# Performance work log

Hardware: AMD Instinct MI355X
Metric: run time of the kernel (lower is better)

Reference implementation:

```python
import math
import jax, jax.numpy as jnp
import numpy as np

N = 50000
C = 128      # in_channels == out_channels
H = 8        # nhead
D = C // H   # head_dim = 16
E = 800000


def _layernorm(x, g, b, eps=1e-5):
    mu = jnp.mean(x, axis=-1, keepdims=True)
    var = jnp.var(x, axis=-1, keepdims=True)
    return (x - mu) * jax.lax.rsqrt(var + eps) * g + b


def setup_inputs() -> dict:
    key = jax.random.key(0)
    ks = jax.random.split(key, 12)
    s = 1.0 / math.sqrt(C)          # ~xavier scale
    s4 = 1.0 / math.sqrt(4 * C)
    return {
        "x": jax.random.normal(ks[0], (N, C), dtype=jnp.float32),
        "edge_index": jax.random.randint(ks[1], (2, E), 0, N, dtype=jnp.int64),
        "Wq": jax.random.normal(ks[2], (C, C), dtype=jnp.float32) * s,
        "Wk": jax.random.normal(ks[3], (C, C), dtype=jnp.float32) * s,
        "Wv": jax.random.normal(ks[4], (C, C), dtype=jnp.float32) * s,
        "Wo": jax.random.normal(ks[5], (C, C), dtype=jnp.float32) * s,
        "bo": jnp.zeros((C,), dtype=jnp.float32),
        "Wf1": jax.random.normal(ks[6], (C, 4 * C), dtype=jnp.float32) * s,
        "bf1": jnp.zeros((4 * C,), dtype=jnp.float32),
        "Wf2": jax.random.normal(ks[7], (4 * C, C), dtype=jnp.float32) * s4,
        "bf2": jnp.zeros((C,), dtype=jnp.float32),
        "g1": jnp.ones((C,), dtype=jnp.float32),
        "b1": jnp.zeros((C,), dtype=jnp.float32),
        "g2": jnp.ones((C,), dtype=jnp.float32),
        "b2": jnp.zeros((C,), dtype=jnp.float32),
    }


def reference(x, edge_index, Wq, Wk, Wv, Wo, bo, Wf1, bf1, Wf2, bf2, g1, b1, g2, b2):
    n = x.shape[0]
    loops = jnp.arange(n, dtype=edge_index.dtype)
    row = jnp.concatenate([edge_index[0], loops])  # source nodes
    col = jnp.concatenate([edge_index[1], loops])  # destination nodes

    q = (x @ Wq).reshape(n, H, D)
    k = (x @ Wk).reshape(n, H, D)
    v = (x @ Wv).reshape(n, H, D)

    # edge-level attention scores [E+N, H]
    scores = jnp.einsum('ehd,ehd->eh', q[row], k[col]) / math.sqrt(D)
    smax = jax.ops.segment_max(scores, col, num_segments=n)  # every node has a self-loop
    exp = jnp.exp(scores - smax[col])
    ssum = jax.ops.segment_sum(exp, col, num_segments=n)
    alpha = exp / (ssum[col] + 1e-8)

    out = jax.ops.segment_sum(v[row] * alpha[..., None], col, num_segments=n)
    attn = out.reshape(n, C) @ Wo + bo

    residual = x  # input_proj is Identity (in_channels == out_channels)
    x1 = _layernorm(residual + attn, g1, b1)
    ffn = jax.nn.gelu(x1 @ Wf1 + bf1, approximate=False) @ Wf2 + bf2
    return _layernorm(x1 + ffn, g2, b2)
```

## Files before the change

kernel.cpp:

```cpp
#include <hip/hip_runtime.h>
#include <cmath>


typedef short bf16x8 __attribute__((ext_vector_type(8)));
typedef float f32x4 __attribute__((ext_vector_type(4)));
typedef unsigned int uint_as1 __attribute__((address_space(1)));
typedef unsigned int uint_as3 __attribute__((address_space(3)));

__device__ inline unsigned short f2bf(float f) {
    unsigned int u = __float_as_uint(f);
    u += 0x7fffu + ((u >> 16) & 1u);
    return (unsigned short)(u >> 16);
}
__device__ inline float bflo(unsigned int w) { return __uint_as_float(w << 16); }
__device__ inline float bfhi(unsigned int w) { return __uint_as_float(w & 0xffff0000u); }

__device__ inline void gload16(const unsigned short* g, unsigned short* l) {
    __builtin_amdgcn_global_load_lds((const uint_as1*)g, (uint_as3*)l, 16, 0, 0);
}

__device__ inline float gelu_f(float x) {
    float ax = fabsf(x) * 0.70710678118f;
    float t = __builtin_amdgcn_rcpf(fmaf(0.3275911f, ax, 1.0f));
    float p = fmaf(1.061405429f, t, -1.453152027f);
    p = fmaf(p, t, 1.421413741f);
    p = fmaf(p, t, -0.284496736f);
    p = fmaf(p, t, 0.254829592f);
    p = p * t;
    float e = __expf(-ax * ax);
    float pe = p * e;
    float w = (x >= 0.f) ? (2.0f - pe) : pe;
    return 0.5f * x * w;
}


__device__ __forceinline__ void stage_panel(unsigned short* Bs,
                                            const unsigned short* base,
                                            int strideK) {
    int tid = threadIdx.x;
    int srow = tid >> 4, cc = tid & 15;
    int gc = (cc & ~7) | ((cc & 7) ^ (srow & 7));
    const unsigned short* src = base + (size_t)srow * strideK + gc * 8;
    unsigned short* dst = Bs + srow * 128 + cc * 8;
#pragma unroll
    for (int j = 0; j < 8; ++j)
        gload16(src + (size_t)j * 16 * strideK, dst + j * 16 * 128);
}

__device__ __forceinline__ void loadA16(bf16x8 (&af)[4],
                                        const unsigned short* A, int M, int K,
                                        int base, int ko, int l16, int quad) {
    int row = base + l16;
    if (row > M - 1) row = M - 1;
    const unsigned short* ar = A + (size_t)row * K + ko + quad * 8;
#pragma unroll
    for (int j = 0; j < 4; ++j) af[j] = *(const bf16x8*)(ar + j * 32);
}

__device__ __forceinline__ void loadA_k(bf16x8 (&af)[4][4],
                                        const unsigned short* A, int M, int K,
                                        int m0, int ko, int wr, int l16, int quad) {
#pragma unroll
    for (int ti = 0; ti < 4; ++ti) {
        int row = m0 + wr * 64 + ti * 16 + l16;
        if (row > M - 1) row = M - 1;
        const unsigned short* ar = A + (size_t)row * K + ko + quad * 8;
#pragma unroll
        for (int j = 0; j < 4; ++j) af[ti][j] = *(const bf16x8*)(ar + j * 32);
    }
}

__device__ __forceinline__ void mm16(f32x4 (&acc)[4][4], const bf16x8 (&af)[4][4],
                                     const unsigned short* Bs,
                                     int wc, int quad, int l16) {
#pragma unroll
    for (int ks = 0; ks < 4; ++ks) {
        bf16x8 bfr[4];
#pragma unroll
        for (int tj = 0; tj < 4; ++tj) {
            int nr = wc * 64 + tj * 16 + l16;
            int cidx = ks * 4 + quad;
            int slot = (cidx & ~7) | ((cidx & 7) ^ (nr & 7));
            bfr[tj] = *(const bf16x8*)&Bs[nr * 128 + slot * 8];
        }
#pragma unroll
        for (int ti = 0; ti < 4; ++ti)
#pragma unroll
            for (int tj = 0; tj < 4; ++tj)
                acc[ti][tj] = __builtin_amdgcn_mfma_f32_16x16x32_bf16(
                    af[ti][ks], bfr[tj], acc[ti][tj], 0, 0, 0);
    }
}


__global__ __launch_bounds__(256) void k_init(
    const float* __restrict__ x, unsigned short* __restrict__ xb,
    const float* __restrict__ Wq, const float* __restrict__ Wk,
    const float* __restrict__ Wv, const float* __restrict__ Wo,
    const float* __restrict__ Wf1, const float* __restrict__ Wf2,
    unsigned short* __restrict__ Wqkvt, unsigned short* __restrict__ Wot,
    unsigned short* __restrict__ Wf1t, unsigned short* __restrict__ Wf2t,
    int* __restrict__ cursor, int4* __restrict__ csrz,
    int N, int nCsr4, int nCast) {
    int bid = blockIdx.x;
    int t = threadIdx.x;

    int NBc = (N + 255) >> 8;
    if (bid < NBc) {
        int i = bid * 256 + t;
        if (i < N) cursor[i] = 0;
        return;
    }
    bid -= NBc;
    int NBz = (nCsr4 + 255) >> 8;
    if (bid < NBz) {
        int i = bid * 256 + t;
        if (i < nCsr4) csrz[i] = make_int4(0, 0, 0, 0);
        return;
    }
    bid -= NBz;
    if (bid < nCast) {
        int i = bid * 256 + t;
        if (i < N * 32) {
            float4 v = ((const float4*)x)[i];
            ushort4 o;
            o.x = f2bf(v.x); o.y = f2bf(v.y); o.z = f2bf(v.z); o.w = f2bf(v.w);
            ((ushort4*)xb)[i] = o;
        }
        return;
    }
    bid -= nCast;
    int z, idx;
    if (bid < 256) { z = bid >> 6; idx = (bid & 63) * 256 + t; }
    else           { z = 4 + ((bid - 256) >> 8); idx = ((bid - 256) & 255) * 256 + t; }

    const float* in; unsigned short* out; int K, Co;
    switch (z) {
        case 0: in = Wq;  out = Wqkvt; K = 128; Co = 128; break;
        case 1: in = Wk;  out = Wqkvt; K = 128; Co = 128; break;
        case 2: in = Wv;  out = Wqkvt; K = 128; Co = 128; break;
        case 3: in = Wo;  out = Wot;   K = 128; Co = 128; break;
        case 4: in = Wf1; out = Wf1t;  K = 128; Co = 512; break;
        default: in = Wf2; out = Wf2t; K = 512; Co = 128; break;
    }
    if (idx >= K * Co) return;
    int k = idx / Co, c = idx % Co;
    int row;
    switch (z) {
        case 0: row = ((c >> 1) << 2) | (c & 1); break;
        case 1: row = 256 + c; break;
        case 2: row = (((c >> 1) << 2) | (c & 1)) + 2; break;
        default: row = c; break;
    }
    out[(size_t)row * K + k] = f2bf(in[idx]);
}


__global__ void k_fill(const int* __restrict__ ei, int* __restrict__ cursor,
                       unsigned short* __restrict__ csr, int E, int N) {
    int e = blockIdx.x * 256 + threadIdx.x;
    if (e >= E + N) return;
    int row, col;
    if (e < E) { row = ei[e]; col = ei[E + e]; }
    else       { row = col = e - E; }
    int pos = atomicAdd(&cursor[col], 1);
    csr[(size_t)col * 64 + pos] = (unsigned short)row;
}


template <int EPI>
__global__ __launch_bounds__(256) void k_gemmP(
    const unsigned short* __restrict__ A, const unsigned short* __restrict__ Bt,
    const float* __restrict__ bias, const float* __restrict__ resid,
    const float* __restrict__ g, const float* __restrict__ b,
    float* __restrict__ outf, unsigned short* __restrict__ outb,
    int M, int Cout, int NZ) {
    __shared__ unsigned short Bs[128 * 128];

    int tid = threadIdx.x;
    int w = tid >> 6, lane = tid & 63;
    int quad = lane >> 4, l16 = lane & 15;
    int zi = blockIdx.x % NZ;
    int ci = blockIdx.x / NZ;
    int n0 = zi * 128;

    stage_panel(Bs, Bt + (size_t)n0 * 128, 128);

    float bi[8], gv[8], bv[8];
    if constexpr (EPI >= 1) {
#pragma unroll
        for (int tj = 0; tj < 8; ++tj) bi[tj] = bias[n0 * (EPI == 1) + tj * 16 + l16];
    }
    if constexpr (EPI == 2) {
#pragma unroll
        for (int tj = 0; tj < 8; ++tj) {
            gv[tj] = g[tj * 16 + l16];
            bv[tj] = b[tj * 16 + l16];
        }
    }

    int base0 = ci * 128 + w * 16;
    int base1 = base0 + 64;
    bf16x8 afA[4], afB[4];
    loadA16(afA, A, M, 128, base0, 0, l16, quad);
    loadA16(afB, A, M, 128, base1, 0, l16, quad);
    __syncthreads();

    auto tile = [&](const bf16x8 (&af)[4], int base) {
        f32x4 acc[8];
#pragma unroll
        for (int tj = 0; tj < 8; ++tj) acc[tj] = {0.f, 0.f, 0.f, 0.f};
#pragma unroll
        for (int ks = 0; ks < 4; ++ks) {
            int cidx = ks * 4 + quad;
#pragma unroll
            for (int tj = 0; tj < 8; ++tj) {
                int nr = tj * 16 + l16;
                int slot = (cidx & ~7) | ((cidx & 7) ^ (nr & 7));
                bf16x8 bfr = *(const bf16x8*)&Bs[nr * 128 + slot * 8];
                acc[tj] = __builtin_amdgcn_mfma_f32_16x16x32_bf16(
                    af[ks], bfr, acc[tj], 0, 0, 0);
            }
        }
        if constexpr (EPI == 0) {
#pragma unroll
            for (int tj = 0; tj < 8; ++tj) {
                int col = n0 + tj * 16 + l16;
#pragma unroll
                for (int r = 0; r < 4; ++r) {
                    int row = base + quad * 4 + r;
                    if (row < M) outb[(size_t)row * Cout + col] = f2bf(acc[tj][r]);
                }
            }
        } else if constexpr (EPI == 1) {
#pragma unroll
            for (int tj = 0; tj < 8; ++tj) {
                int col = n0 + tj * 16 + l16;
#pragma unroll
                for (int r = 0; r < 4; ++r) {
                    int row = base + quad * 4 + r;
                    if (row < M)
                        outb[(size_t)row * Cout + col] = f2bf(gelu_f(acc[tj][r] + bi[tj]));
                }
            }
        } else {
#pragma unroll
            for (int tj = 0; tj < 8; ++tj) {
                int col = tj * 16 + l16;
#pragma unroll
                for (int r = 0; r < 4; ++r) {
                    int row = base + quad * 4 + r;
                    float rv = (row < M) ? resid[(size_t)row * 128 + col] : 0.f;
                    acc[tj][r] += bi[tj] + rv;
                }
            }
#pragma unroll
            for (int r = 0; r < 4; ++r) {
                float s = 0.f, q = 0.f;
#pragma unroll
                for (int tj = 0; tj < 8; ++tj) {
                    s += acc[tj][r];
                    q += acc[tj][r] * acc[tj][r];
                }
                s += __shfl_xor(s, 1); q += __shfl_xor(q, 1);
                s += __shfl_xor(s, 2); q += __shfl_xor(q, 2);
                s += __shfl_xor(s, 4); q += __shfl_xor(q, 4);
                s += __shfl_xor(s, 8); q += __shfl_xor(q, 8);
                float mean = s * 0.0078125f;
                float var = q * 0.0078125f - mean * mean;
                float rs = rsqrtf(var + 1e-5f);
                int row = base + quad * 4 + r;
                bool ok = row < M;
#pragma unroll
                for (int tj = 0; tj < 8; ++tj) {
                    int col = tj * 16 + l16;
                    float y = (acc[tj][r] - mean) * rs * gv[tj] + bv[tj];
                    if (ok) {
                        outf[(size_t)row * 128 + col] = y;
                        outb[(size_t)row * 128 + col] = f2bf(y);
                    }
                }
            }
        }
    };

    tile(afA, base0);
    tile(afB, base1);
}


template <int KT>
__global__ __launch_bounds__(256) void k_gemmK(
    const unsigned short* __restrict__ A, const unsigned short* __restrict__ Bt,
    const float* __restrict__ bias, const float* __restrict__ resid,
    const float* __restrict__ g, const float* __restrict__ b,
    float* __restrict__ outf, int M) {
    constexpr int K = KT * 128;
    __shared__ unsigned short smem[128 * 128];
    __shared__ float pS[2][128], pQ[2][128];

    int tid = threadIdx.x;
    int wid = tid >> 6, lane = tid & 63;
    int quad = lane >> 4, l16 = lane & 15;
    int wr = wid >> 1, wc = wid & 1;
    int m0 = blockIdx.x * 128;

    f32x4 acc[4][4];
#pragma unroll
    for (int i = 0; i < 4; ++i)
#pragma unroll
        for (int j = 0; j < 4; ++j) acc[i][j] = {0.f, 0.f, 0.f, 0.f};

#pragma unroll
    for (int kt = 0; kt < KT; ++kt) {
        bf16x8 af[4][4];
        loadA_k(af, A, M, K, m0, kt * 128, wr, l16, quad);
        stage_panel(smem, Bt + kt * 128, K);
        __syncthreads();
        mm16(acc, af, smem, wc, quad, l16);
        __syncthreads();
    }

    float bi[4], gv[4], bv[4];
#pragma unroll
    for (int tj = 0; tj < 4; ++tj) {
        int col = wc * 64 + tj * 16 + l16;
        bi[tj] = bias[col]; gv[tj] = g[col]; bv[tj] = b[col];
    }
#pragma unroll
    for (int ti = 0; ti < 4; ++ti)
#pragma unroll
        for (int tj = 0; tj < 4; ++tj) {
            int col = wc * 64 + tj * 16 + l16;
#pragma unroll
            for (int r = 0; r < 4; ++r) {
                int row = m0 + wr * 64 + ti * 16 + quad * 4 + r;
                float rv = (row < M) ? resid[(size_t)row * 128 + col] : 0.f;
                acc[ti][tj][r] += bi[tj] + rv;
            }
        }
#pragma unroll
    for (int ti = 0; ti < 4; ++ti)
#pragma unroll
        for (int r = 0; r < 4; ++r) {
            float s = acc[ti][0][r] + acc[ti][1][r] + acc[ti][2][r] + acc[ti][3][r];
            float q = acc[ti][0][r] * acc[ti][0][r] + acc[ti][1][r] * acc[ti][1][r]
                    + acc[ti][2][r] * acc[ti][2][r] + acc[ti][3][r] * acc[ti][3][r];
            s += __shfl_xor(s, 1); q += __shfl_xor(q, 1);
            s += __shfl_xor(s, 2); q += __shfl_xor(q, 2);
            s += __shfl_xor(s, 4); q += __shfl_xor(q, 4);
            s += __shfl_xor(s, 8); q += __shfl_xor(q, 8);
            if (l16 == 0) {
                int lr = wr * 64 + ti * 16 + quad * 4 + r;
                pS[wc][lr] = s; pQ[wc][lr] = q;
            }
        }
    __syncthreads();
    if (tid < 128) {
        float s = pS[0][tid] + pS[1][tid];
        float q = pQ[0][tid] + pQ[1][tid];
        float mean = s * 0.0078125f;
        float var = q * 0.0078125f - mean * mean;
        pS[0][tid] = mean;
        pQ[0][tid] = rsqrtf(var + 1e-5f);
    }
    __syncthreads();
#pragma unroll
    for (int ti = 0; ti < 4; ++ti)
#pragma unroll
        for (int r = 0; r < 4; ++r) {
            int lr = wr * 64 + ti * 16 + quad * 4 + r;
            int row = m0 + lr;
            if (row >= M) continue;
            float mean = pS[0][lr], rs = pQ[0][lr];
#pragma unroll
            for (int tj = 0; tj < 4; ++tj) {
                int col = wc * 64 + tj * 16 + l16;
                outf[(size_t)row * 128 + col] =
                    (acc[ti][tj][r] - mean) * rs * gv[tj] + bv[tj];
            }
        }
}


__global__ __launch_bounds__(256) void k_attn(
    const unsigned int* __restrict__ qkv, const int* __restrict__ counts,
    const unsigned short* __restrict__ csr, unsigned int* __restrict__ ob,
    int N) {
    int j = blockIdx.x * 4 + (threadIdx.x >> 6);
    if (j >= N) return;
    int l = threadIdx.x & 63;
    int lk = l & 31;
    int half = l >> 5;
    const uint4* qv4 = (const uint4*)qkv;

    uint2 kw = *(const uint2*)(qkv + (size_t)j * 192 + 128 + lk * 2);
    const float S = 0.36067376022224085f;
    float k0 = bflo(kw.x) * S, k1 = bfhi(kw.x) * S;
    float k2 = bflo(kw.y) * S, k3 = bfhi(kw.y) * S;

    int cnt = counts[j];
    int nb = (cnt + 3) >> 2;
    const unsigned short* cp = csr + (size_t)j * 64;

    int ra0 = cp[half],     rb0 = cp[2 + half];
    int ra1 = cp[4 + half], rb1 = cp[6 + half];
    uint4 gA = qv4[(unsigned)ra0 * 48u + lk];
    uint4 gB = qv4[(unsigned)rb0 * 48u + lk];

    float lsum = 0.f, a0 = 0.f, a1 = 0.f, a2 = 0.f, a3 = 0.f;
    for (int bi = 0; bi < nb; ++bi) {
        int ra2 = cp[(bi + 2) * 4 + half];
        int rb2 = cp[(bi + 2) * 4 + 2 + half];
        uint4 nA = qv4[(unsigned)ra1 * 48u + lk];
        uint4 nB = qv4[(unsigned)rb1 * 48u + lk];

        int rem = cnt - bi * 4;
        {
            float s = fmaf(bflo(gA.x), k0,
                      fmaf(bfhi(gA.x), k1,
                      fmaf(bflo(gA.z), k2, bfhi(gA.z) * k3)));
            s += __shfl_xor(s, 1);
            s += __shfl_xor(s, 2);
            float e = exp2f(s);
            e = (half < rem) ? e : 0.f;
            lsum += e;
            a0 = fmaf(e, bflo(gA.y), a0); a1 = fmaf(e, bfhi(gA.y), a1);
            a2 = fmaf(e, bflo(gA.w), a2); a3 = fmaf(e, bfhi(gA.w), a3);
        }
        {
            float s = fmaf(bflo(gB.x), k0,
                      fmaf(bfhi(gB.x), k1,
                      fmaf(bflo(gB.z), k2, bfhi(gB.z) * k3)));
            s += __shfl_xor(s, 1);
            s += __shfl_xor(s, 2);
            float e = exp2f(s);
            e = (2 + half < rem) ? e : 0.f;
            lsum += e;
            a0 = fmaf(e, bflo(gB.y), a0); a1 = fmaf(e, bfhi(gB.y), a1);
            a2 = fmaf(e, bflo(gB.w), a2); a3 = fmaf(e, bfhi(gB.w), a3);
        }
        gA = nA; gB = nB; ra1 = ra2; rb1 = rb2;
    }

    lsum += __shfl_xor(lsum, 32);
    a0 += __shfl_xor(a0, 32); a1 += __shfl_xor(a1, 32);
    a2 += __shfl_xor(a2, 32); a3 += __shfl_xor(a3, 32);

    if (half == 0) {
        float inv = 1.f / (lsum + 1e-8f);
        uint2 o;
        o.x = ((unsigned int)f2bf(a1 * inv) << 16) | (unsigned int)f2bf(a0 * inv);
        o.y = ((unsigned int)f2bf(a3 * inv) << 16) | (unsigned int)f2bf(a2 * inv);
        *(uint2*)(ob + (size_t)j * 64 + lk * 2) = o;
    }
}


extern "C" void kernel_launch(void* const* d_in, const int* in_sizes, int n_in,
                              void* d_out, int out_size, void* d_ws, size_t ws_size,
                              hipStream_t stream) {
    const float* x   = (const float*)d_in[0];
    const int* ei    = (const int*)d_in[1];
    const float* Wq  = (const float*)d_in[2];
    const float* Wk  = (const float*)d_in[3];
    const float* Wv  = (const float*)d_in[4];
    const float* Wo  = (const float*)d_in[5];
    const float* bo  = (const float*)d_in[6];
    const float* Wf1 = (const float*)d_in[7];
    const float* bf1 = (const float*)d_in[8];
    const float* Wf2 = (const float*)d_in[9];
    const float* bf2 = (const float*)d_in[10];
    const float* g1  = (const float*)d_in[11];
    const float* b1  = (const float*)d_in[12];
    const float* g2  = (const float*)d_in[13];
    const float* b2  = (const float*)d_in[14];

    int N = in_sizes[0] / 128;
    int E = in_sizes[1] / 2;
    int N2 = ((N + 127) / 128) * 128;
    int NE = E + N;

    char* p = (char*)d_ws;
    auto alloc = [&](size_t bytes) -> char* {
        char* r = p;
        p += (bytes + 255) & ~(size_t)255;
        return r;
    };
    unsigned short* qkv = (unsigned short*)alloc((size_t)N2 * 512 * 2);
    unsigned short* ob  = qkv + (size_t)N2 * 384;
    unsigned short* hb  = qkv;
    unsigned short* x1b = (unsigned short*)alloc((size_t)N2 * 128 * 2);
    unsigned short* xb  = x1b;
    float* x1f          = (float*)alloc((size_t)N2 * 128 * 4);
    unsigned short* Wqkvt = (unsigned short*)alloc(384 * 128 * 2);
    unsigned short* Wot   = (unsigned short*)alloc(128 * 128 * 2);
    unsigned short* Wf1t  = (unsigned short*)alloc(512 * 128 * 2);
    unsigned short* Wf2t  = (unsigned short*)alloc(128 * 512 * 2);
    int* cursor = (int*)alloc((size_t)N * 4);
    unsigned short* csr = (unsigned short*)alloc(((size_t)N * 64 + 256) * 2);

    int nCsr4 = N * 8 + 32;
    int nCast = (N * 32 + 255) / 256;
    int nInit = ((N + 255) / 256) + ((nCsr4 + 255) / 256) + nCast + 768;
    int M128 = (N + 127) / 128;

    k_init<<<nInit, 256, 0, stream>>>(x, xb, Wq, Wk, Wv, Wo, Wf1, Wf2,
                                      Wqkvt, Wot, Wf1t, Wf2t,
                                      cursor, (int4*)csr, N, nCsr4, nCast);
    k_fill<<<(NE + 255) / 256, 256, 0, stream>>>(ei, cursor, csr, E, N);

    k_gemmP<0><<<3 * M128, 256, 0, stream>>>(
        xb, Wqkvt, nullptr, nullptr, nullptr, nullptr, nullptr, qkv,
        N, 384, 3);

    k_attn<<<(N + 3) / 4, 256, 0, stream>>>((const unsigned int*)qkv, cursor,
                                            csr, (unsigned int*)ob, N);

    k_gemmP<2><<<M128, 256, 0, stream>>>(
        ob, Wot, bo, x, g1, b1, x1f, x1b, N, 128, 1);

    k_gemmP<1><<<4 * M128, 256, 0, stream>>>(
        x1b, Wf1t, bf1, nullptr, nullptr, nullptr, nullptr, hb, N, 512, 4);

    k_gemmK<4><<<M128, 256, 0, stream>>>(
        hb, Wf2t, bf2, x1f, g2, b2, (float*)d_out, N);
}
```

Before: 319.8 us.

## Drop CSR zeroing, partition fill by column range, persistent attention with deeper prefetch

The CSR buffer is no longer zero-filled. Out-of-range neighbor slots are instead guarded in the attention kernel, which substitutes index 0. The fill kernel now runs eight passes over all edges, each handling one column range, to improve locality of the atomics and scattered CSR writes, at the cost of re-reading the edge list eight times. The attention kernel becomes a grid-stride persistent kernel with 2048 blocks and prefetches one more neighbor batch ahead to hide gather latency.

```diff
diff --git a/kernel.cpp b/kernel.cpp
--- a/kernel.cpp
+++ b/kernel.cpp
@@ -100,8 +100,7 @@
     const float* __restrict__ Wf1, const float* __restrict__ Wf2,
     unsigned short* __restrict__ Wqkvt, unsigned short* __restrict__ Wot,
     unsigned short* __restrict__ Wf1t, unsigned short* __restrict__ Wf2t,
-    int* __restrict__ cursor, int4* __restrict__ csrz,
-    int N, int nCsr4, int nCast) {
+    int* __restrict__ cursor, int N, int nCast) {
     int bid = blockIdx.x;
     int t = threadIdx.x;
 
@@ -112,13 +111,6 @@
         return;
     }
     bid -= NBc;
-    int NBz = (nCsr4 + 255) >> 8;
-    if (bid < NBz) {
-        int i = bid * 256 + t;
-        if (i < nCsr4) csrz[i] = make_int4(0, 0, 0, 0);
-        return;
-    }
-    bid -= NBz;
     if (bid < nCast) {
         int i = bid * 256 + t;
         if (i < N * 32) {
@@ -157,12 +149,15 @@
 
 
 __global__ void k_fill(const int* __restrict__ ei, int* __restrict__ cursor,
-                       unsigned short* __restrict__ csr, int E, int N) {
-    int e = blockIdx.x * 256 + threadIdx.x;
+                       unsigned short* __restrict__ csr, int E, int N,
+                       int NB, int Rng) {
+    int pass = blockIdx.x / NB;
+    int e = (blockIdx.x - pass * NB) * 256 + threadIdx.x;
     if (e >= E + N) return;
-    int row, col;
-    if (e < E) { row = ei[e]; col = ei[E + e]; }
-    else       { row = col = e - E; }
+    int lo = pass * Rng, hi = lo + Rng;
+    int col = (e < E) ? ei[E + e] : (e - E);
+    if (col < lo || col >= hi) return;
+    int row = (e < E) ? ei[e] : col;
     int pos = atomicAdd(&cursor[col], 1);
     csr[(size_t)col * 64 + pos] = (unsigned short)row;
 }
@@ -387,72 +382,82 @@
     const unsigned int* __restrict__ qkv, const int* __restrict__ counts,
     const unsigned short* __restrict__ csr, unsigned int* __restrict__ ob,
     int N) {
-    int j = blockIdx.x * 4 + (threadIdx.x >> 6);
-    if (j >= N) return;
     int l = threadIdx.x & 63;
     int lk = l & 31;
     int half = l >> 5;
     const uint4* qv4 = (const uint4*)qkv;
-
-    uint2 kw = *(const uint2*)(qkv + (size_t)j * 192 + 128 + lk * 2);
     const float S = 0.36067376022224085f;
-    float k0 = bflo(kw.x) * S, k1 = bfhi(kw.x) * S;
-    float k2 = bflo(kw.y) * S, k3 = bfhi(kw.y) * S;
-
-    int cnt = counts[j];
-    int nb = (cnt + 3) >> 2;
-    const unsigned short* cp = csr + (size_t)j * 64;
-
-    int ra0 = cp[half],     rb0 = cp[2 + half];
-    int ra1 = cp[4 + half], rb1 = cp[6 + half];
-    uint4 gA = qv4[(unsigned)ra0 * 48u + lk];
-    uint4 gB = qv4[(unsigned)rb0 * 48u + lk];
-
-    float lsum = 0.f, a0 = 0.f, a1 = 0.f, a2 = 0.f, a3 = 0.f;
-    for (int bi = 0; bi < nb; ++bi) {
-        int ra2 = cp[(bi + 2) * 4 + half];
-        int rb2 = cp[(bi + 2) * 4 + 2 + half];
-        uint4 nA = qv4[(unsigned)ra1 * 48u + lk];
-        uint4 nB = qv4[(unsigned)rb1 * 48u + lk];
-
-        int rem = cnt - bi * 4;
-        {
-            float s = fmaf(bflo(gA.x), k0,
-                      fmaf(bfhi(gA.x), k1,
-                      fmaf(bflo(gA.z), k2, bfhi(gA.z) * k3)));
-            s += __shfl_xor(s, 1);
-            s += __shfl_xor(s, 2);
-            float e = exp2f(s);
-            e = (half < rem) ? e : 0.f;
-            lsum += e;
-            a0 = fmaf(e, bflo(gA.y), a0); a1 = fmaf(e, bfhi(gA.y), a1);
-            a2 = fmaf(e, bflo(gA.w), a2); a3 = fmaf(e, bfhi(gA.w), a3);
-        }
-        {
-            float s = fmaf(bflo(gB.x), k0,
-                      fmaf(bfhi(gB.x), k1,
-                      fmaf(bflo(gB.z), k2, bfhi(gB.z) * k3)));
-            s += __shfl_xor(s, 1);
-            s += __shfl_xor(s, 2);
-            float e = exp2f(s);
-            e = (2 + half < rem) ? e : 0.f;
-            lsum += e;
-            a0 = fmaf(e, bflo(gB.y), a0); a1 = fmaf(e, bfhi(gB.y), a1);
-            a2 = fmaf(e, bflo(gB.w), a2); a3 = fmaf(e, bfhi(gB.w), a3);
-        }
-        gA = nA; gB = nB; ra1 = ra2; rb1 = rb2;
-    }
-
-    lsum += __shfl_xor(lsum, 32);
-    a0 += __shfl_xor(a0, 32); a1 += __shfl_xor(a1, 32);
-    a2 += __shfl_xor(a2, 32); a3 += __shfl_xor(a3, 32);
-
-    if (half == 0) {
-        float inv = 1.f / (lsum + 1e-8f);
-        uint2 o;
-        o.x = ((unsigned int)f2bf(a1 * inv) << 16) | (unsigned int)f2bf(a0 * inv);
-        o.y = ((unsigned int)f2bf(a3 * inv) << 16) | (unsigned int)f2bf(a2 * inv);
-        *(uint2*)(ob + (size_t)j * 64 + lk * 2) = o;
+    int W = gridDim.x * 4;
+
+    for (int j = blockIdx.x * 4 + (threadIdx.x >> 6); j < N; j += W) {
+        uint2 kw = *(const uint2*)(qkv + (size_t)j * 192 + 128 + lk * 2);
+        float k0 = bflo(kw.x) * S, k1 = bfhi(kw.x) * S;
+        float k2 = bflo(kw.y) * S, k3 = bfhi(kw.y) * S;
+
+        int cnt = counts[j];
+        int nb = (cnt + 3) >> 2;
+        const unsigned short* cp = csr + (size_t)j * 64;
+
+        int i0a = cp[half];
+        int i0b = (2 + half < cnt) ? cp[2 + half] : 0;
+        int i1a = (4 + half < cnt) ? cp[4 + half] : 0;
+        int i1b = (6 + half < cnt) ? cp[6 + half] : 0;
+        uint4 g0A = qv4[(unsigned)i0a * 48u + lk];
+        uint4 g0B = qv4[(unsigned)i0b * 48u + lk];
+        uint4 g1A = qv4[(unsigned)i1a * 48u + lk];
+        uint4 g1B = qv4[(unsigned)i1b * 48u + lk];
+        int i2a = (8 + half < cnt) ? cp[8 + half] : 0;
+        int i2b = (10 + half < cnt) ? cp[10 + half] : 0;
+
+        float lsum = 0.f, a0 = 0.f, a1 = 0.f, a2 = 0.f, a3 = 0.f;
+        for (int bi = 0; bi < nb; ++bi) {
+            uint4 g2A = qv4[(unsigned)i2a * 48u + lk];
+            uint4 g2B = qv4[(unsigned)i2b * 48u + lk];
+            int s3 = (bi + 3) * 4;
+            i2a = (s3 + half < cnt) ? cp[s3 + half] : 0;
+            i2b = (s3 + 2 + half < cnt) ? cp[s3 + 2 + half] : 0;
+
+            int rem = cnt - bi * 4;
+            {
+                float s = fmaf(bflo(g0A.x), k0,
+                          fmaf(bfhi(g0A.x), k1,
+                          fmaf(bflo(g0A.z), k2, bfhi(g0A.z) * k3)));
+                s += __shfl_xor(s, 1);
+                s += __shfl_xor(s, 2);
+                float e = exp2f(s);
+                e = (half < rem) ? e : 0.f;
+                lsum += e;
+                a0 = fmaf(e, bflo(g0A.y), a0); a1 = fmaf(e, bfhi(g0A.y), a1);
+                a2 = fmaf(e, bflo(g0A.w), a2); a3 = fmaf(e, bfhi(g0A.w), a3);
+            }
+            {
+                float s = fmaf(bflo(g0B.x), k0,
+                          fmaf(bfhi(g0B.x), k1,
+                          fmaf(bflo(g0B.z), k2, bfhi(g0B.z) * k3)));
+                s += __shfl_xor(s, 1);
+                s += __shfl_xor(s, 2);
+                float e = exp2f(s);
+                e = (2 + half < rem) ? e : 0.f;
+                lsum += e;
+                a0 = fmaf(e, bflo(g0B.y), a0); a1 = fmaf(e, bfhi(g0B.y), a1);
+                a2 = fmaf(e, bflo(g0B.w), a2); a3 = fmaf(e, bfhi(g0B.w), a3);
+            }
+            g0A = g1A; g0B = g1B; g1A = g2A; g1B = g2B;
+        }
+
+        float ls = lsum + __shfl_xor(lsum, 32);
+        float b0 = a0 + __shfl_xor(a0, 32);
+        float b1 = a1 + __shfl_xor(a1, 32);
+        float b2 = a2 + __shfl_xor(a2, 32);
+        float b3 = a3 + __shfl_xor(a3, 32);
+
+        if (half == 0) {
+            float inv = 1.f / (ls + 1e-8f);
+            uint2 o;
+            o.x = ((unsigned int)f2bf(b1 * inv) << 16) | (unsigned int)f2bf(b0 * inv);
+            o.y = ((unsigned int)f2bf(b3 * inv) << 16) | (unsigned int)f2bf(b2 * inv);
+            *(uint2*)(ob + (size_t)j * 64 + lk * 2) = o;
+        }
     }
 }
 
@@ -500,22 +505,23 @@
     int* cursor = (int*)alloc((size_t)N * 4);
     unsigned short* csr = (unsigned short*)alloc(((size_t)N * 64 + 256) * 2);
 
-    int nCsr4 = N * 8 + 32;
     int nCast = (N * 32 + 255) / 256;
-    int nInit = ((N + 255) / 256) + ((nCsr4 + 255) / 256) + nCast + 768;
+    int nInit = ((N + 255) / 256) + nCast + 768;
     int M128 = (N + 127) / 128;
+    int NB = (NE + 255) / 256;
+    int Rng = (N + 7) / 8;
 
     k_init<<<nInit, 256, 0, stream>>>(x, xb, Wq, Wk, Wv, Wo, Wf1, Wf2,
                                       Wqkvt, Wot, Wf1t, Wf2t,
-                                      cursor, (int4*)csr, N, nCsr4, nCast);
-    k_fill<<<(NE + 255) / 256, 256, 0, stream>>>(ei, cursor, csr, E, N);
+                                      cursor, N, nCast);
+    k_fill<<<8 * NB, 256, 0, stream>>>(ei, cursor, csr, E, N, NB, Rng);
 
     k_gemmP<0><<<3 * M128, 256, 0, stream>>>(
         xb, Wqkvt, nullptr, nullptr, nullptr, nullptr, nullptr, qkv,
         N, 384, 3);
 
-    k_attn<<<(N + 3) / 4, 256, 0, stream>>>((const unsigned int*)qkv, cursor,
-                                            csr, (unsigned int*)ob, N);
+    k_attn<<<2048, 256, 0, stream>>>((const unsigned int*)qkv, cursor,
+                                     csr, (unsigned int*)ob, N);
 
     k_gemmP<2><<<M128, 256, 0, stream>>>(
         ob, Wot, bo, x, g1, b1, x1f, x1b, N, 128, 1);
```

New measurement: 324.9 us. No clear change (+1.6%).
